# Optimization experiments

Measured on AMD Instinct MI355X. Metric: run time of the kernel, lower is better.

Reference implementation:

```python
import jax, jax.numpy as jnp
import numpy as np

IGNORE = 255
DSN_W = 0.4
AFF_W = 1.0
NUM_CLASSES = 19
CITYSCAPES_W = np.array([0.8373, 0.918, 0.866, 1.0345, 1.0166, 0.9969, 0.9754, 1.0489,
                         0.8786, 1.0023, 0.9539, 0.9843, 1.1116, 0.9037, 1.0865, 1.0955,
                         1.0865, 1.1529, 1.0507], dtype=np.float32)


def _nearest_downsample(label, ph, pw):
    # PyTorch F.upsample(mode='nearest'): src_idx = floor(dst_idx * in/out)
    B, H, W = label.shape
    ri = (jnp.arange(ph) * H) // ph
    ci = (jnp.arange(pw) * W) // pw
    return label[:, ri][:, :, ci]


def _weighted_ce(logits, target, weight):
    # logits [B,C,H,W], target [B,H,W]; class-weighted CE with ignore_index
    logp = jax.nn.log_softmax(logits, axis=1)
    mask = (target != IGNORE)
    safe = jnp.where(mask, target, 0)
    nll = -jnp.take_along_axis(logp, safe[:, None], axis=1)[:, 0]  # [B,H,W]
    w = weight[safe] * mask.astype(logits.dtype)
    return jnp.sum(w * nll) / jnp.sum(w)


def setup_inputs() -> dict:
    key = jax.random.key(0)
    k1, k2, k3, k4 = jax.random.split(key, 4)
    B, H, W = 1, 768, 768
    ph, pw = 96, 96
    return {
        "aff_pred": jax.random.normal(k1, (B, ph * pw, ph * pw), dtype=jnp.float32),
        "logits1": jax.random.normal(k2, (B, NUM_CLASSES, ph, pw), dtype=jnp.float32),
        "logits2": jax.random.normal(k3, (B, NUM_CLASSES, ph, pw), dtype=jnp.float32),
        "class_weight": jnp.asarray(CITYSCAPES_W),
        "target": jax.random.randint(k4, (B, H, W), 0, NUM_CLASSES, dtype=jnp.int32),
    }


def reference(aff_pred, logits1, logits2, class_weight, target):
    B, H, W = target.shape
    ph, pw = logits2.shape[2], logits2.shape[3]
    # Affinity branch: nearest-downsample labels, pairwise equality, MSE
    lab = _nearest_downsample(target, ph, pw).reshape(B, ph * pw).astype(jnp.float32)
    aff_gt = (lab[:, :, None] == lab[:, None, :]).astype(jnp.float32)  # [B, N, N]
    aff_loss = jnp.mean((aff_pred - aff_gt) ** 2)
    # CE branches: bilinear upsample (align_corners=False, i.e. half-pixel)
    sp1 = jax.image.resize(logits1, (B, logits1.shape[1], H, W), method='bilinear')
    loss1 = _weighted_ce(sp1, target, class_weight)
    sp2 = jax.image.resize(logits2, (B, logits2.shape[1], H, W), method='bilinear')
    loss2 = _weighted_ce(sp2, target, class_weight)
    return DSN_W * loss1 + loss2 + AFF_W * aff_loss
```

## Files before the change

### kernel.cpp

```cpp
#include <hip/hip_runtime.h>
#include <math.h>

#define NPIX   9216
#define PH     96
#define FULL_H 768
#define NC     19
#define IGN    255

#define AFF_ROWS   4
#define AFF_BLOCKS (NPIX / AFF_ROWS)
#define CE_BLOCKS  ((FULL_H * FULL_H) / 256)
#define FUSED_BLOCKS (AFF_BLOCKS + CE_BLOCKS)


__device__ __forceinline__ float block_reduce_f(float v, float* sm) {
    #pragma unroll
    for (int o = 32; o > 0; o >>= 1) v += __shfl_down(v, o, 64);
    int lane = threadIdx.x & 63, wid = threadIdx.x >> 6;
    if (lane == 0) sm[wid] = v;
    __syncthreads();
    if (threadIdx.x == 0) v = sm[0] + sm[1] + sm[2] + sm[3];
    return v;
}

__device__ __forceinline__ double block_reduce_d(double v, double* sm) {
    #pragma unroll
    for (int o = 32; o > 0; o >>= 1) v += __shfl_down(v, o, 64);
    int lane = threadIdx.x & 63, wid = threadIdx.x >> 6;
    if (lane == 0) sm[wid] = v;
    __syncthreads();
    if (threadIdx.x == 0) v = sm[0] + sm[1] + sm[2] + sm[3];
    return v;
}

__global__ __launch_bounds__(256) void prep_kernel(const int* __restrict__ target,
                                                   int* __restrict__ lab) {
    int i = blockIdx.x * 256 + threadIdx.x;
    if (i < NPIX) {
        int r = i / PH, c = i % PH;
        lab[i] = target[(r * 8) * FULL_H + c * 8];
    }
}

__device__ __forceinline__ float aff_term(float4 p, int4 l, int ln) {
    float d0 = p.x - (l.x == ln ? 1.f : 0.f);
    float d1 = p.y - (l.y == ln ? 1.f : 0.f);
    float d2 = p.z - (l.z == ln ? 1.f : 0.f);
    float d3 = p.w - (l.w == ln ? 1.f : 0.f);
    return d0 * d0 + d1 * d1 + d2 * d2 + d3 * d3;
}

__global__ __launch_bounds__(256) void fused_kernel(const float* __restrict__ aff,
                                                    const int* __restrict__ lab,
                                                    const float* __restrict__ lg1,
                                                    const float* __restrict__ lg2,
                                                    const float* __restrict__ cw,
                                                    const int* __restrict__ target,
                                                    float* __restrict__ aff_part,
                                                    float* __restrict__ p1,
                                                    float* __restrict__ p2,
                                                    float* __restrict__ pd) {
    __shared__ float sm[4];
    const int bid = blockIdx.x;

    if ((bid & 1) == 0) {
        const int grp = bid >> 1;
        const int r0 = grp * AFF_ROWS;
        const int ln0 = lab[r0 + 0], ln1 = lab[r0 + 1];
        const int ln2 = lab[r0 + 2], ln3 = lab[r0 + 3];
        const float4* rp = (const float4*)(aff + (size_t)r0 * NPIX);
        const int4*   lp = (const int4*)lab;
        float s = 0.f;
        #pragma unroll
        for (int k = threadIdx.x; k < NPIX / 4; k += 256) {
            int4   l  = lp[k];
            float4 q0 = rp[k + 0 * (NPIX / 4)];
            float4 q1 = rp[k + 1 * (NPIX / 4)];
            float4 q2 = rp[k + 2 * (NPIX / 4)];
            float4 q3 = rp[k + 3 * (NPIX / 4)];
            s += aff_term(q0, l, ln0);
            s += aff_term(q1, l, ln1);
            s += aff_term(q2, l, ln2);
            s += aff_term(q3, l, ln3);
        }
        s = block_reduce_f(s, sm);
        if (threadIdx.x == 0) aff_part[grp] = s;
    } else {
        const int grp = bid >> 1;
        const int idx = grp * 256 + threadIdx.x;
        float num1 = 0.f, num2 = 0.f, den = 0.f;

        const int h = idx / FULL_H, w = idx - h * FULL_H;
        const int t = target[idx];
        if (t != IGN) {
            float py = (h + 0.5f) * 0.125f - 0.5f;
            float px = (w + 0.5f) * 0.125f - 0.5f;
            int y0 = (int)floorf(py); float fy = py - (float)y0;
            int x0 = (int)floorf(px); float fx = px - (float)x0;
            int y1 = min(y0 + 1, PH - 1); y0 = max(y0, 0);
            int x1 = min(x0 + 1, PH - 1); x0 = max(x0, 0);
            const float w00 = (1.f - fx) * (1.f - fy), w10 = fx * (1.f - fy);
            const float w01 = (1.f - fx) * fy,         w11 = fx * fy;
            const int o00 = y0 * PH + x0, o10 = y0 * PH + x1;
            const int o01 = y1 * PH + x0, o11 = y1 * PH + x1;

            float se1 = 0.f, se2 = 0.f, vt1 = 0.f, vt2 = 0.f;
            #pragma unroll
            for (int c = 0; c < NC; ++c) {
                const float* b1 = lg1 + c * NPIX;
                const float* b2 = lg2 + c * NPIX;
                float v1 = w00 * b1[o00] + w10 * b1[o10] + w01 * b1[o01] + w11 * b1[o11];
                float v2 = w00 * b2[o00] + w10 * b2[o10] + w01 * b2[o01] + w11 * b2[o11];
                se1 += __expf(v1);
                se2 += __expf(v2);
                if (c == t) { vt1 = v1; vt2 = v2; }
            }
            const float wt = cw[t];
            num1 = wt * (__logf(se1) - vt1);
            num2 = wt * (__logf(se2) - vt2);
            den  = wt;
        }

        float r1 = block_reduce_f(num1, sm); __syncthreads();
        float r2 = block_reduce_f(num2, sm); __syncthreads();
        float rd = block_reduce_f(den,  sm);
        if (threadIdx.x == 0) {
            p1[grp] = r1;
            p2[grp] = r2;
            pd[grp] = rd;
        }
    }
}

__global__ __launch_bounds__(256) void final_kernel(const float* __restrict__ aff_part,
                                                    const float* __restrict__ p1,
                                                    const float* __restrict__ p2,
                                                    const float* __restrict__ pd,
                                                    float* __restrict__ out) {
    __shared__ double sm[4];
    double sa = 0.0, s1 = 0.0, s2 = 0.0, sd = 0.0;
    for (int i = threadIdx.x; i < AFF_BLOCKS; i += 256) sa += (double)aff_part[i];
    for (int i = threadIdx.x; i < CE_BLOCKS; i += 256) {
        s1 += (double)p1[i];
        s2 += (double)p2[i];
        sd += (double)pd[i];
    }
    double ra = block_reduce_d(sa, sm); __syncthreads();
    double r1 = block_reduce_d(s1, sm); __syncthreads();
    double r2 = block_reduce_d(s2, sm); __syncthreads();
    double rd = block_reduce_d(sd, sm);
    if (threadIdx.x == 0) {
        double aff = ra / ((double)NPIX * (double)NPIX);
        double l1  = r1 / rd;
        double l2  = r2 / rd;
        out[0] = (float)(0.4 * l1 + l2 + 1.0 * aff);
    }
}

extern "C" void kernel_launch(void* const* d_in, const int* in_sizes, int n_in,
                              void* d_out, int out_size, void* d_ws, size_t ws_size,
                              hipStream_t stream) {
    const float* aff_pred = (const float*)d_in[0];
    const float* logits1  = (const float*)d_in[1];
    const float* logits2  = (const float*)d_in[2];
    const float* cw       = (const float*)d_in[3];
    const int*   target   = (const int*)d_in[4];
    float* out = (float*)d_out;

    char* ws = (char*)d_ws;
    int*   lab      = (int*)ws;
    float* aff_part = (float*)(ws + 36864);
    float* ce1      = (float*)(ws + 36864 +  9216);
    float* ce2      = (float*)(ws + 36864 + 18432);
    float* ced      = (float*)(ws + 36864 + 27648);

    prep_kernel<<<(NPIX + 255) / 256, 256, 0, stream>>>(target, lab);
    fused_kernel<<<FUSED_BLOCKS, 256, 0, stream>>>(aff_pred, lab, logits1, logits2, cw,
                                                   target, aff_part, ce1, ce2, ced);
    final_kernel<<<1, 256, 0, stream>>>(aff_part, ce1, ce2, ced, out);
}
```

Baseline: 90.55 us.

## Process eight affinity rows per block and make CE blocks persistent over tiles

Each affinity block now handles eight rows instead of four, so every label vector load serves more rows and there are half as many blocks. The CE work is placed in 256 blocks that each loop over nine pixel tiles and accumulate locally, instead of one block per tile interleaved with the affinity blocks. Affinity blocks now come first in the grid, and the final reduction reads only 256 CE partials. The risks are higher register pressure from eight in-flight float4 loads, and CE blocks being scheduled last, which could leave a tail of long-running blocks.

```diff
diff --git a/kernel.cpp b/kernel.cpp
--- a/kernel.cpp
+++ b/kernel.cpp
@@ -7,10 +7,15 @@
 #define NC     19
 #define IGN    255
 
-#define AFF_ROWS   4
+#define AFF_ROWS   8
 #define AFF_BLOCKS (NPIX / AFF_ROWS)
-#define CE_BLOCKS  ((FULL_H * FULL_H) / 256)
+#define CE_TILES   ((FULL_H * FULL_H) / 256)
+#define CE_BLOCKS  256
+#define CE_PER_BLK (CE_TILES / CE_BLOCKS)
 #define FUSED_BLOCKS (AFF_BLOCKS + CE_BLOCKS)
+
+typedef float f4 __attribute__((ext_vector_type(4)));
+typedef int   i4 __attribute__((ext_vector_type(4)));
 
 
 __device__ __forceinline__ float block_reduce_f(float v, float* sm) {
@@ -42,7 +47,7 @@
     }
 }
 
-__device__ __forceinline__ float aff_term(float4 p, int4 l, int ln) {
+__device__ __forceinline__ float aff_term(f4 p, i4 l, int ln) {
     float d0 = p.x - (l.x == ln ? 1.f : 0.f);
     float d1 = p.y - (l.y == ln ? 1.f : 0.f);
     float d2 = p.z - (l.z == ln ? 1.f : 0.f);
@@ -63,71 +68,71 @@
     __shared__ float sm[4];
     const int bid = blockIdx.x;
 
-    if ((bid & 1) == 0) {
-        const int grp = bid >> 1;
-        const int r0 = grp * AFF_ROWS;
-        const int ln0 = lab[r0 + 0], ln1 = lab[r0 + 1];
-        const int ln2 = lab[r0 + 2], ln3 = lab[r0 + 3];
-        const float4* rp = (const float4*)(aff + (size_t)r0 * NPIX);
-        const int4*   lp = (const int4*)lab;
+    if (bid < AFF_BLOCKS) {
+        const int r0 = bid * AFF_ROWS;
+        int ln[AFF_ROWS];
+        #pragma unroll
+        for (int j = 0; j < AFF_ROWS; ++j) ln[j] = lab[r0 + j];
+        const f4* rp = (const f4*)(aff + (size_t)r0 * NPIX);
+        const i4* lp = (const i4*)lab;
         float s = 0.f;
         #pragma unroll
         for (int k = threadIdx.x; k < NPIX / 4; k += 256) {
-            int4   l  = lp[k];
-            float4 q0 = rp[k + 0 * (NPIX / 4)];
-            float4 q1 = rp[k + 1 * (NPIX / 4)];
-            float4 q2 = rp[k + 2 * (NPIX / 4)];
-            float4 q3 = rp[k + 3 * (NPIX / 4)];
-            s += aff_term(q0, l, ln0);
-            s += aff_term(q1, l, ln1);
-            s += aff_term(q2, l, ln2);
-            s += aff_term(q3, l, ln3);
+            i4 l = lp[k];
+            f4 q[AFF_ROWS];
+            #pragma unroll
+            for (int j = 0; j < AFF_ROWS; ++j) q[j] = rp[k + j * (NPIX / 4)];
+            #pragma unroll
+            for (int j = 0; j < AFF_ROWS; ++j) s += aff_term(q[j], l, ln[j]);
         }
         s = block_reduce_f(s, sm);
-        if (threadIdx.x == 0) aff_part[grp] = s;
+        if (threadIdx.x == 0) aff_part[bid] = s;
     } else {
-        const int grp = bid >> 1;
-        const int idx = grp * 256 + threadIdx.x;
+        const int cb = bid - AFF_BLOCKS;
         float num1 = 0.f, num2 = 0.f, den = 0.f;
 
-        const int h = idx / FULL_H, w = idx - h * FULL_H;
-        const int t = target[idx];
-        if (t != IGN) {
-            float py = (h + 0.5f) * 0.125f - 0.5f;
-            float px = (w + 0.5f) * 0.125f - 0.5f;
-            int y0 = (int)floorf(py); float fy = py - (float)y0;
-            int x0 = (int)floorf(px); float fx = px - (float)x0;
-            int y1 = min(y0 + 1, PH - 1); y0 = max(y0, 0);
-            int x1 = min(x0 + 1, PH - 1); x0 = max(x0, 0);
-            const float w00 = (1.f - fx) * (1.f - fy), w10 = fx * (1.f - fy);
-            const float w01 = (1.f - fx) * fy,         w11 = fx * fy;
-            const int o00 = y0 * PH + x0, o10 = y0 * PH + x1;
-            const int o01 = y1 * PH + x0, o11 = y1 * PH + x1;
+        #pragma unroll
+        for (int it = 0; it < CE_PER_BLK; ++it) {
+            const int idx = (cb + it * CE_BLOCKS) * 256 + threadIdx.x;
+            const int h = idx / FULL_H, w = idx - h * FULL_H;
+            const int t = target[idx];
+            if (t != IGN) {
+                float py = (h + 0.5f) * 0.125f - 0.5f;
+                float px = (w + 0.5f) * 0.125f - 0.5f;
+                int y0 = (int)floorf(py); float fy = py - (float)y0;
+                int x0 = (int)floorf(px); float fx = px - (float)x0;
+                int y1 = min(y0 + 1, PH - 1); y0 = max(y0, 0);
+                int x1 = min(x0 + 1, PH - 1); x0 = max(x0, 0);
+                const float w00 = (1.f - fx) * (1.f - fy), w10 = fx * (1.f - fy);
+                const float w01 = (1.f - fx) * fy,         w11 = fx * fy;
+                const int o00 = y0 * PH + x0, o10 = y0 * PH + x1;
+                const int o01 = y1 * PH + x0, o11 = y1 * PH + x1;
 
-            float se1 = 0.f, se2 = 0.f, vt1 = 0.f, vt2 = 0.f;
-            #pragma unroll
-            for (int c = 0; c < NC; ++c) {
-                const float* b1 = lg1 + c * NPIX;
-                const float* b2 = lg2 + c * NPIX;
-                float v1 = w00 * b1[o00] + w10 * b1[o10] + w01 * b1[o01] + w11 * b1[o11];
-                float v2 = w00 * b2[o00] + w10 * b2[o10] + w01 * b2[o01] + w11 * b2[o11];
-                se1 += __expf(v1);
-                se2 += __expf(v2);
-                if (c == t) { vt1 = v1; vt2 = v2; }
+                float se1 = 0.f, se2 = 0.f, vt1 = 0.f, vt2 = 0.f;
+                #pragma unroll
+                for (int c = 0; c < NC; ++c) {
+                    const float* b1 = lg1 + c * NPIX;
+                    const float* b2 = lg2 + c * NPIX;
+                    float v1 = w00 * b1[o00] + w10 * b1[o10] + w01 * b1[o01] + w11 * b1[o11];
+                    float v2 = w00 * b2[o00] + w10 * b2[o10] + w01 * b2[o01] + w11 * b2[o11];
+                    se1 += __expf(v1);
+                    se2 += __expf(v2);
+                    if (c == t) { vt1 = v1; vt2 = v2; }
+                }
+                const float wt = cw[t];
+                num1 += wt * (__logf(se1) - vt1);
+                num2 += wt * (__logf(se2) - vt2);
+                den  += wt;
             }
-            const float wt = cw[t];
-            num1 = wt * (__logf(se1) - vt1);
-            num2 = wt * (__logf(se2) - vt2);
-            den  = wt;
         }
 
         float r1 = block_reduce_f(num1, sm); __syncthreads();
         float r2 = block_reduce_f(num2, sm); __syncthreads();
         float rd = block_reduce_f(den,  sm);
         if (threadIdx.x == 0) {
-            p1[grp] = r1;
-            p2[grp] = r2;
-            pd[grp] = rd;
+            p1[cb] = r1;
+            p2[cb] = r2;
+            pd[cb] = rd;
         }
     }
 }
@@ -140,10 +145,10 @@
     __shared__ double sm[4];
     double sa = 0.0, s1 = 0.0, s2 = 0.0, sd = 0.0;
     for (int i = threadIdx.x; i < AFF_BLOCKS; i += 256) sa += (double)aff_part[i];
-    for (int i = threadIdx.x; i < CE_BLOCKS; i += 256) {
-        s1 += (double)p1[i];
-        s2 += (double)p2[i];
-        sd += (double)pd[i];
+    if (threadIdx.x < CE_BLOCKS) {
+        s1 = (double)p1[threadIdx.x];
+        s2 = (double)p2[threadIdx.x];
+        sd = (double)pd[threadIdx.x];
     }
     double ra = block_reduce_d(sa, sm); __syncthreads();
     double r1 = block_reduce_d(s1, sm); __syncthreads();
@@ -170,9 +175,9 @@
     char* ws = (char*)d_ws;
     int*   lab      = (int*)ws;
     float* aff_part = (float*)(ws + 36864);
-    float* ce1      = (float*)(ws + 36864 +  9216);
-    float* ce2      = (float*)(ws + 36864 + 18432);
-    float* ced      = (float*)(ws + 36864 + 27648);
+    float* ce1      = (float*)(ws + 41472);
+    float* ce2      = (float*)(ws + 42496);
+    float* ced      = (float*)(ws + 43520);
 
     prep_kernel<<<(NPIX + 255) / 256, 256, 0, stream>>>(target, lab);
     fused_kernel<<<FUSED_BLOCKS, 256, 0, stream>>>(aff_pred, lab, logits1, logits2, cw,
```

After: 93.22 us. 1.03x slower.
